# Kernel tuning notes

Hardware: AMD Instinct MI355X
Metric: run time of the kernel (lower is better)

## Reference

```python
import jax, jax.numpy as jnp
import numpy as np

N_NODES = 50000
N_EDGES = 800000
N_GRAPHS = 64


def setup_inputs() -> dict:
    key = jax.random.key(0)
    ks = jax.random.split(key, 12)

    def w(k, shape):
        fan_in = shape[0]
        return jax.random.normal(k, shape, dtype=jnp.float32) / np.sqrt(fan_in)

    x = jax.random.normal(ks[0], (N_NODES, 6), dtype=jnp.float32)
    edge_index = jax.random.randint(ks[1], (2, N_EDGES), 0, N_NODES, dtype=jnp.int64)
    batch = jnp.sort(jax.random.randint(ks[2], (N_NODES,), 0, N_GRAPHS, dtype=jnp.int64))
    return {
        "x": x,
        "edge_index": edge_index,
        "batch": batch,
        "W_in": w(ks[3], (6, 64)),
        "b_in": jnp.zeros((64,), jnp.float32),
        "W1": w(ks[4], (64, 128)),
        "b1": jnp.zeros((128,), jnp.float32),
        "W2": w(ks[5], (128, 128)),
        "b2": jnp.zeros((128,), jnp.float32),
        "Wp": w(ks[6], (256, 256)),
        "bp": jnp.zeros((256,), jnp.float32),
    }


def reference(x, edge_index, batch, W_in, b_in, W1, b1, W2, b2, Wp, bp):
    n = x.shape[0]
    self_loop = jnp.arange(n, dtype=edge_index.dtype)
    src = jnp.concatenate([edge_index[0], self_loop])  # [E+N]
    dst = jnp.concatenate([edge_index[1], self_loop])
    # GCN symmetric normalization with self-loops (PyG GCNConv default)
    deg = jax.ops.segment_sum(jnp.ones_like(dst, x.dtype), dst, num_segments=n)
    dinv = jax.lax.rsqrt(deg)  # deg >= 1 because of self-loops
    norm = (dinv[src] * dinv[dst])[:, None]  # [E+N, 1]

    def gcn(h, W, b):
        hw = h @ W                       # linear first, like GCNConv
        msg = hw[src] * norm             # gather + normalize per edge
        return jax.ops.segment_sum(msg, dst, num_segments=n) + b

    h = x @ W_in + b_in                  # input_projection
    h = jax.nn.relu(gcn(h, W1, b1))      # relu(gnn1(...))
    h = jax.nn.relu(gcn(h, W2, b2))      # relu(gnn2(...))

    # global mean / max pooling over batch segments
    counts = jax.ops.segment_sum(jnp.ones((n,), h.dtype), batch, num_segments=N_GRAPHS)
    h_mean = jax.ops.segment_sum(h, batch, num_segments=N_GRAPHS) / jnp.maximum(counts, 1.0)[:, None]
    h_max = jax.ops.segment_max(h, batch, num_segments=N_GRAPHS)
    h_max = jnp.where(counts[:, None] > 0, h_max, 0.0)
    h_graph = jnp.concatenate([h_mean, h_max], axis=1)  # [G, 256]

    # projection MLP: Linear + ReLU (Dropout is identity in eval)
    return jax.nn.relu(h_graph @ Wp + bp)
```

## Files before the change

### kernel.cpp

```cpp
#include <hip/hip_runtime.h>
#include <hip/hip_fp16.h>

#define N_NODES 50000
#define N_EDGES 800000
#define N_GRAPHS 64
#define N_PAD 50048

#define CB 256
#define EPB (N_EDGES / CB)
#define NBUCKET ((N_NODES + 255) / 256)

typedef _Float16 f16x8 __attribute__((ext_vector_type(8)));
typedef float f32x4 __attribute__((ext_vector_type(4)));

__device__ __forceinline__ unsigned splice2(unsigned z) {
    return ((z & 0x80u) << 8) | ((z & 0x7fu) << 7) |
           ((z & 0x8000u) << 16) | ((z & 0x7f00u) << 15);
}
__device__ __forceinline__ f16x8 dec8(uint2 w) {
    union { unsigned u[4]; f16x8 v; } o;
    o.u[0] = splice2(w.x);
    o.u[1] = splice2(w.x >> 16);
    o.u[2] = splice2(w.y);
    o.u[3] = splice2(w.y >> 16);
    return o.v;
}


__global__ void k_prep(const float* __restrict__ W_in, const float* __restrict__ b_in,
                       const float* __restrict__ W1, const float* __restrict__ W2,
                       _Float16* __restrict__ Wt2, float* __restrict__ Wcz,
                       float* psum, float* pmax, int* totals, int* gcursor,
                       const int* __restrict__ batch, float* __restrict__ pcnt) {
    int idx = blockIdx.x * blockDim.x + threadIdx.x;
    if (idx < 128 * 128) {
        int n = idx >> 7, k = idx & 127;
        Wt2[idx] = (_Float16)(W2[k * 128 + n] * 8.0f);
    } else if (idx < 128 * 128 + 1024) {
        int j = idx - 128 * 128;
        int ch = j >> 3, k = j & 7;
        float acc = 0.f;
        if (k < 6) {
            for (int q = 0; q < 64; q++) acc += W_in[k * 64 + q] * W1[q * 128 + ch];
        } else if (k == 6) {
            for (int q = 0; q < 64; q++) acc += b_in[q] * W1[q * 128 + ch];
        }
        Wcz[k * 128 + ch] = acc;
    }
    if (idx < N_GRAPHS * 128) { psum[idx] = 0.f; pmax[idx] = 0.f; }
    if (idx < 256) { totals[idx] = 0; gcursor[idx] = 0; }
    if (blockIdx.x == 0) {
        __shared__ int shp[N_GRAPHS + 1];
        int tt = threadIdx.x;
        if (tt <= N_GRAPHS) {
            int lo = 0, hi = N_NODES;
            while (lo < hi) {
                int mid = (lo + hi) >> 1;
                if (batch[mid] < tt) lo = mid + 1; else hi = mid;
            }
            shp[tt] = lo;
        }
        __syncthreads();
        if (tt < N_GRAPHS) pcnt[tt] = (float)(shp[tt + 1] - shp[tt]);
    }
}


__global__ __launch_bounds__(256) void k_coarse_hist(const int* __restrict__ dst,
                                                     int* __restrict__ totals) {
    __shared__ int hist[NBUCKET];
    int t = threadIdx.x, b = blockIdx.x;
    for (int i = t; i < NBUCKET; i += 256) hist[i] = 0;
    __syncthreads();
    int e0 = b * EPB;
    for (int e = e0 + t; e < e0 + EPB; e += 256)
        atomicAdd(&hist[dst[e] >> 8], 1);
    __syncthreads();
    for (int i = t; i < NBUCKET; i += 256)
        if (hist[i] > 0) atomicAdd(&totals[i], hist[i]);
}

__global__ __launch_bounds__(256) void k_scan_scatter(
        const int* __restrict__ src, const int* __restrict__ dst,
        const int* __restrict__ totals, int* __restrict__ bucket_base,
        int* __restrict__ gcursor, unsigned int* __restrict__ esort) {
    __shared__ int cur[256];
    __shared__ int sc[256];
    int t = threadIdx.x, b = blockIdx.x;
    cur[t] = 0;
    __syncthreads();
    int e0 = b * EPB;
    for (int e = e0 + t; e < e0 + EPB; e += 256)
        atomicAdd(&cur[dst[e] >> 8], 1);
    __syncthreads();
    int lcnt = cur[t];
    int v = (t < NBUCKET) ? totals[t] : 0;
    sc[t] = v;
    __syncthreads();
    for (int off = 1; off < 256; off <<= 1) {
        int u = (t >= off) ? sc[t - off] : 0;
        __syncthreads();
        sc[t] += u;
        __syncthreads();
    }
    int base = sc[t] - v;
    int off = (t < NBUCKET && lcnt > 0) ? atomicAdd(&gcursor[t], lcnt) : 0;
    cur[t] = base + off;
    if (b == 0) {
        if (t < NBUCKET) bucket_base[t] = base;
        if (t == 0) bucket_base[NBUCKET] = N_EDGES;
    }
    __syncthreads();
    for (int e = e0 + t; e < e0 + EPB; e += 256) {
        int d = dst[e];
        int slot = atomicAdd(&cur[d >> 8], 1);
        esort[slot] = ((unsigned)(d & 255) << 16) | (unsigned)src[e];
    }
}

__global__ __launch_bounds__(256) void k_fine_fill_p(
        const unsigned int* __restrict__ esort, const int* __restrict__ bucket_base,
        int* __restrict__ col, int* __restrict__ row_ptr, float* __restrict__ dinv,
        const float* __restrict__ x, float* __restrict__ p) {
    __shared__ int hist[256];
    __shared__ int sc[256];
    __shared__ int cur[256];
    int t = threadIdx.x, b = blockIdx.x;
    hist[t] = 0;
    __syncthreads();
    int base = bucket_base[b], end = bucket_base[b + 1];
    for (int e = base + t; e < end; e += 256)
        atomicAdd(&hist[(esort[e] >> 16) & 255], 1);
    __syncthreads();
    int v = hist[t];
    sc[t] = v;
    __syncthreads();
    for (int off = 1; off < 256; off <<= 1) {
        int u = (t >= off) ? sc[t - off] : 0;
        __syncthreads();
        sc[t] += u;
        __syncthreads();
    }
    int start = base + sc[t] - v;
    cur[t] = start;
    int node = b * 256 + t;
    float di = rsqrtf((float)(v + 1));
    if (node < N_NODES) {
        row_ptr[node] = start;
        dinv[node] = di;
        float pr[8];
#pragma unroll
        for (int k = 0; k < 6; k++) pr[k] = x[node * 6 + k] * di;
        pr[6] = di;
        pr[7] = 0.f;
        *(f32x4*)&p[(size_t)node * 8] = *(f32x4*)&pr[0];
        *(f32x4*)&p[(size_t)node * 8 + 4] = *(f32x4*)&pr[4];
    }
    if (b == 0 && t == 0) row_ptr[N_NODES] = N_EDGES;
    __syncthreads();
    for (int e = base + t; e < end; e += 256) {
        unsigned pk = esort[e];
        int slot = atomicAdd(&cur[(pk >> 16) & 255], 1);
        col[slot] = (int)(pk & 0xffffu);
    }
}

__global__ __launch_bounds__(256, 8) void k_agg_proj(
        const float* __restrict__ p, const int* __restrict__ row_ptr,
        const int* __restrict__ col, const float* __restrict__ Wcz,
        const float* __restrict__ b1, const float* __restrict__ dinv,
        unsigned char* __restrict__ g1, int n) {
    __shared__ float tl[32][8];
    __shared__ float Wl[8 * 128];
    __shared__ float bl[128];
    int t = threadIdx.x;
    for (int i = t; i < 1024; i += 256) Wl[i] = Wcz[i];
    if (t < 128) bl[t] = b1[t];

    int rg = t >> 3, ck = t & 7;
    int row = blockIdx.x * 32 + rg;
    float acc = 0.f;
    if (row < n) {
        acc = p[(size_t)row * 8 + ck];
        int e = row_ptr[row], e1 = row_ptr[row + 1];
        for (; e + 3 < e1; e += 4) {
            int c0 = col[e], c1 = col[e + 1], c2 = col[e + 2], c3 = col[e + 3];
            float v0 = p[(size_t)c0 * 8 + ck];
            float v1 = p[(size_t)c1 * 8 + ck];
            float v2 = p[(size_t)c2 * 8 + ck];
            float v3 = p[(size_t)c3 * 8 + ck];
            acc += (v0 + v1) + (v2 + v3);
        }
        for (; e < e1; e++) acc += p[(size_t)col[e] * 8 + ck];
    }
    tl[rg][ck] = acc;
    __syncthreads();

    int rg2 = t >> 3, oc = t & 7;
    int row2 = blockIdx.x * 32 + rg2;
    if (row2 < n) {
        float tr[7];
#pragma unroll
        for (int k = 0; k < 7; k++) tr[k] = tl[rg2][k];
        float di = dinv[row2];
        unsigned w[4] = {0u, 0u, 0u, 0u};
#pragma unroll
        for (int c = 0; c < 16; c++) {
            int ch = oc * 16 + c;
            float z = 0.f;
#pragma unroll
            for (int k = 0; k < 7; k++) z += tr[k] * Wl[k * 128 + ch];
            z = di * z + bl[ch];
            float h = fmaxf(z, 0.f) * di;
            union { _Float16 f; unsigned short u; } cv;
            cv.f = (_Float16)(h * 0.125f);
            unsigned hb = cv.u;
            unsigned r = hb & 0x7fffu;
            r = r + 0x3fu + ((r >> 7) & 1u);
            unsigned byte = ((hb >> 8) & 0x80u) | ((r >> 7) & 0x7fu);
            w[c >> 2] |= byte << ((c & 3) * 8);
        }
        *(uint4*)&g1[(size_t)row2 * 128 + oc * 16] = make_uint4(w[0], w[1], w[2], w[3]);
    }
}

__global__ __launch_bounds__(256, 8) void k_gnn2f8(
        const unsigned char* __restrict__ g, const int* __restrict__ row_ptr,
        const int* __restrict__ col, const _Float16* __restrict__ Wt2,
        const float* __restrict__ b2, const float* __restrict__ dinv,
        const int* __restrict__ batch, float* __restrict__ psum,
        float* __restrict__ pmax, int n) {
    constexpr int ROWS = 16, KP = 136;
    __shared__ __align__(16) char smem[ROWS * 128 * 4];
    _Float16* Sl = (_Float16*)smem;
    float* Hs = (float*)smem;
    int t = threadIdx.x;

    {
        int rl = t >> 4, ck = t & 15;
        int row = blockIdx.x * ROWS + rl;
        f16x8 accA = {};
        f16x8 accB = {};
        const uint2* gb = (const uint2*)g;
        if (row < n) {
            accA = dec8(gb[(size_t)row * 16 + ck]);
            int e = row_ptr[row], e1 = row_ptr[row + 1];
            for (; e + 3 < e1; e += 4) {
                int c0 = col[e], c1 = col[e + 1], c2 = col[e + 2], c3 = col[e + 3];
                uint2 v0 = gb[(size_t)c0 * 16 + ck];
                uint2 v1 = gb[(size_t)c1 * 16 + ck];
                uint2 v2 = gb[(size_t)c2 * 16 + ck];
                uint2 v3 = gb[(size_t)c3 * 16 + ck];
                accA += dec8(v0);
                accB += dec8(v1);
                accA += dec8(v2);
                accB += dec8(v3);
            }
            if (e + 1 < e1) {
                uint2 v0 = gb[(size_t)col[e] * 16 + ck];
                uint2 v1 = gb[(size_t)col[e + 1] * 16 + ck];
                accA += dec8(v0);
                accB += dec8(v1);
                e += 2;
            }
            if (e < e1) accA += dec8(gb[(size_t)col[e] * 16 + ck]);
        }
        f16x8 o = accA + accB;
        *(f16x8*)&Sl[rl * KP + ck * 8] = o;
    }
    __syncthreads();

    int wave = t >> 6;
    int lane = t & 63;
    int m = lane & 15;
    int quad = lane >> 4;
    int col_base = wave * 32;

    f32x4 acc[2] = {};
#pragma unroll
    for (int k0 = 0; k0 < 128; k0 += 32) {
        f16x8 a = *(const f16x8*)&Sl[m * KP + k0 + quad * 8];
#pragma unroll
        for (int ct = 0; ct < 2; ct++) {
            f16x8 bw = *(const f16x8*)(Wt2 + (size_t)(col_base + ct * 16 + m) * 128
                                       + k0 + quad * 8);
            acc[ct] = __builtin_amdgcn_mfma_f32_16x16x32_f16(a, bw, acc[ct], 0, 0, 0);
        }
    }

    __syncthreads();
#pragma unroll
    for (int r = 0; r < 4; r++) {
        int rl = quad * 4 + r;
        int row = blockIdx.x * ROWS + rl;
        float di = (row < n) ? dinv[row] : 0.f;
#pragma unroll
        for (int ct = 0; ct < 2; ct++) {
            int colb = col_base + ct * 16 + m;
            float v = fmaxf(di * acc[ct][r] + b2[colb], 0.f);
            Hs[rl * 128 + colb] = (row < n) ? v : 0.f;
        }
    }
    __syncthreads();
    if (t < 128) {
        int colb = t;
        int row0b = blockIdx.x * ROWS;
        float s = 0.f, mx = 0.f;
        int gcur = batch[row0b < n ? row0b : (n - 1)];
        for (int rr = 0; rr < ROWS; rr++) {
            int row = row0b + rr;
            if (row >= n) break;
            int gi = batch[row];
            if (gi != gcur) {
                atomicAdd(&psum[gcur * 128 + colb], s);
                atomicMax((int*)&pmax[gcur * 128 + colb], __float_as_int(mx));
                s = 0.f; mx = 0.f; gcur = gi;
            }
            float v = Hs[rr * 128 + colb];
            s += v;
            mx = fmaxf(mx, v);
        }
        atomicAdd(&psum[gcur * 128 + colb], s);
        atomicMax((int*)&pmax[gcur * 128 + colb], __float_as_int(mx));
    }
}


__global__ void k_final(const float* __restrict__ psum, const float* __restrict__ pmax,
                        const float* __restrict__ pcnt, const float* __restrict__ Wp,
                        const float* __restrict__ bp, float* __restrict__ out) {
    int t = blockIdx.x * blockDim.x + threadIdx.x;
    if (t >= N_GRAPHS * 256) return;
    int g = t >> 8, j = t & 255;
    float inv = 1.0f / fmaxf(pcnt[g], 1.0f);
    float acc = bp[j];
#pragma unroll 4
    for (int k = 0; k < 128; k++) acc += (psum[g * 128 + k] * inv) * Wp[k * 256 + j];
#pragma unroll 4
    for (int k = 0; k < 128; k++) acc += pmax[g * 128 + k] * Wp[(128 + k) * 256 + j];
    out[t] = fmaxf(acc, 0.f);
}

extern "C" void kernel_launch(void* const* d_in, const int* in_sizes, int n_in,
                              void* d_out, int out_size, void* d_ws, size_t ws_size,
                              hipStream_t stream) {
    const int N = N_NODES, E = N_EDGES;
    const float* x    = (const float*)d_in[0];
    const int*   ei   = (const int*)d_in[1];
    const int*   src  = ei;
    const int*   dst  = ei + E;
    const int*   batch= (const int*)d_in[2];
    const float* W_in = (const float*)d_in[3];
    const float* b_in = (const float*)d_in[4];
    const float* W1   = (const float*)d_in[5];
    const float* b1   = (const float*)d_in[6];
    const float* W2   = (const float*)d_in[7];
    const float* b2   = (const float*)d_in[8];
    const float* Wp   = (const float*)d_in[9];
    const float* bp   = (const float*)d_in[10];
    float* out = (float*)d_out;

    char* p8 = (char*)d_ws;
    int* totals      = (int*)p8;   p8 += 256 * 4;
    int* bucket_base = (int*)p8;   p8 += 256 * 4;
    int* gcursor     = (int*)p8;   p8 += 256 * 4;
    int* row_ptr     = (int*)p8;   p8 += (N_PAD + 64) * 4;
    int* col         = (int*)p8;   p8 += (size_t)N_EDGES * 4;
    unsigned* esort  = (unsigned*)p8; p8 += (size_t)N_EDGES * 4;
    float* dinv      = (float*)p8; p8 += N_PAD * 4;
    float* Wcz       = (float*)p8; p8 += 1024 * 4;
    _Float16* Wt2    = (_Float16*)p8; p8 += 128 * 128 * 2;
    float* pfeat     = (float*)p8; p8 += (size_t)N_PAD * 8 * 4;
    unsigned char* g1f8 = (unsigned char*)p8; p8 += (size_t)N_PAD * 128;
    float* psum      = (float*)p8; p8 += N_GRAPHS * 128 * 4;
    float* pmax      = (float*)p8; p8 += N_GRAPHS * 128 * 4;
    float* pcnt      = (float*)p8;

    const int TB = 256;
    dim3 blk(TB);

    k_prep<<<(128 * 128 + 1024 + TB - 1) / TB, blk, 0, stream>>>(
        W_in, b_in, W1, W2, Wt2, Wcz, psum, pmax, totals, gcursor, batch, pcnt);

    k_coarse_hist<<<CB, blk, 0, stream>>>(dst, totals);
    k_scan_scatter<<<CB, blk, 0, stream>>>(src, dst, totals, bucket_base, gcursor, esort);
    k_fine_fill_p<<<NBUCKET, blk, 0, stream>>>(esort, bucket_base, col, row_ptr, dinv,
                                               x, pfeat);

    k_agg_proj<<<(N + 31) / 32, blk, 0, stream>>>(pfeat, row_ptr, col, Wcz, b1, dinv,
                                                  g1f8, N);

    k_gnn2f8<<<(N + 15) / 16, blk, 0, stream>>>(
        g1f8, row_ptr, col, Wt2, b2, dinv, batch, psum, pmax, N);

    k_final<<<(N_GRAPHS * 256 + TB - 1) / TB, blk, 0, stream>>>(psum, pmax, pcnt, Wp, bp, out);
}
```

Baseline: 193.0 us.

## Replace two-pass global edge bucketing with per-block local sort and segment gather

Merges the coarse histogram and scan/scatter kernels into one kernel. Each block sorts its edge chunk by coarse bucket in shared memory, writes it back contiguously, and records per-bucket local offsets. The fine-fill kernel then finds each bucket's segments across all blocks using a prefix scan plus a binary search per edge. This removes one kernel launch, a second pass over dst, the global cursor atomics and scattered global writes, but adds per-edge binary-search overhead and reads from 256 small segments per bucket.

Measured after the change: 202.1 us. 4.7% more time.

```diff
diff --git a/kernel.cpp b/kernel.cpp
--- a/kernel.cpp
+++ b/kernel.cpp
@@ -30,7 +30,7 @@
 __global__ void k_prep(const float* __restrict__ W_in, const float* __restrict__ b_in,
                        const float* __restrict__ W1, const float* __restrict__ W2,
                        _Float16* __restrict__ Wt2, float* __restrict__ Wcz,
-                       float* psum, float* pmax, int* totals, int* gcursor,
+                       float* psum, float* pmax, int* totals,
                        const int* __restrict__ batch, float* __restrict__ pcnt) {
     int idx = blockIdx.x * blockDim.x + threadIdx.x;
     if (idx < 128 * 128) {
@@ -48,7 +48,7 @@
         Wcz[k * 128 + ch] = acc;
     }
     if (idx < N_GRAPHS * 128) { psum[idx] = 0.f; pmax[idx] = 0.f; }
-    if (idx < 256) { totals[idx] = 0; gcursor[idx] = 0; }
+    if (idx < 256) totals[idx] = 0;
     if (blockIdx.x == 0) {
         __shared__ int shp[N_GRAPHS + 1];
         int tt = threadIdx.x;
@@ -65,36 +65,22 @@
     }
 }
 
-
-__global__ __launch_bounds__(256) void k_coarse_hist(const int* __restrict__ dst,
-                                                     int* __restrict__ totals) {
-    __shared__ int hist[NBUCKET];
+__global__ __launch_bounds__(256) void k_lsort(
+        const int* __restrict__ src, const int* __restrict__ dst,
+        int* __restrict__ totals, unsigned int* __restrict__ esort,
+        int* __restrict__ lstart) {
+    __shared__ int hist[256];
+    __shared__ int sc[256];
+    __shared__ int cur[256];
+    __shared__ unsigned stage[EPB];
     int t = threadIdx.x, b = blockIdx.x;
-    for (int i = t; i < NBUCKET; i += 256) hist[i] = 0;
+    hist[t] = 0;
     __syncthreads();
     int e0 = b * EPB;
     for (int e = e0 + t; e < e0 + EPB; e += 256)
         atomicAdd(&hist[dst[e] >> 8], 1);
     __syncthreads();
-    for (int i = t; i < NBUCKET; i += 256)
-        if (hist[i] > 0) atomicAdd(&totals[i], hist[i]);
-}
-
-__global__ __launch_bounds__(256) void k_scan_scatter(
-        const int* __restrict__ src, const int* __restrict__ dst,
-        const int* __restrict__ totals, int* __restrict__ bucket_base,
-        int* __restrict__ gcursor, unsigned int* __restrict__ esort) {
-    __shared__ int cur[256];
-    __shared__ int sc[256];
-    int t = threadIdx.x, b = blockIdx.x;
-    cur[t] = 0;
-    __syncthreads();
-    int e0 = b * EPB;
-    for (int e = e0 + t; e < e0 + EPB; e += 256)
-        atomicAdd(&cur[dst[e] >> 8], 1);
-    __syncthreads();
-    int lcnt = cur[t];
-    int v = (t < NBUCKET) ? totals[t] : 0;
+    int v = hist[t];
     sc[t] = v;
     __syncthreads();
     for (int off = 1; off < 256; off <<= 1) {
@@ -104,33 +90,74 @@
         __syncthreads();
     }
     int base = sc[t] - v;
-    int off = (t < NBUCKET && lcnt > 0) ? atomicAdd(&gcursor[t], lcnt) : 0;
-    cur[t] = base + off;
-    if (b == 0) {
-        if (t < NBUCKET) bucket_base[t] = base;
-        if (t == 0) bucket_base[NBUCKET] = N_EDGES;
-    }
+    cur[t] = base;
+    if (t < NBUCKET) {
+        lstart[t * 256 + b] = base;
+        if (v > 0) atomicAdd(&totals[t], v);
+    }
+    if (t == 0) lstart[NBUCKET * 256 + b] = EPB;
     __syncthreads();
     for (int e = e0 + t; e < e0 + EPB; e += 256) {
         int d = dst[e];
         int slot = atomicAdd(&cur[d >> 8], 1);
-        esort[slot] = ((unsigned)(d & 255) << 16) | (unsigned)src[e];
-    }
+        stage[slot] = ((unsigned)(d & 255) << 16) | (unsigned)src[e];
+    }
+    __syncthreads();
+    for (int i = t; i < EPB; i += 256)
+        esort[e0 + i] = stage[i];
 }
 
 __global__ __launch_bounds__(256) void k_fine_fill_p(
-        const unsigned int* __restrict__ esort, const int* __restrict__ bucket_base,
-        int* __restrict__ col, int* __restrict__ row_ptr, float* __restrict__ dinv,
+        const unsigned int* __restrict__ esort, const int* __restrict__ lstart,
+        const int* __restrict__ totals, int* __restrict__ col,
+        int* __restrict__ row_ptr, float* __restrict__ dinv,
         const float* __restrict__ x, float* __restrict__ p) {
     __shared__ int hist[256];
     __shared__ int sc[256];
     __shared__ int cur[256];
-    int t = threadIdx.x, b = blockIdx.x;
+    __shared__ int segls[256];
+    __shared__ int segoff[257];
+    __shared__ int bb0;
+    int t = threadIdx.x, i = blockIdx.x;
+
+    int tv = (t < NBUCKET) ? totals[t] : 0;
+    sc[t] = tv;
+    __syncthreads();
+    for (int off = 1; off < 256; off <<= 1) {
+        int u = (t >= off) ? sc[t - off] : 0;
+        __syncthreads();
+        sc[t] += u;
+        __syncthreads();
+    }
+    if (t == i) bb0 = sc[t] - tv;
+    int ls = lstart[i * 256 + t];
+    int cnt = lstart[(i + 1) * 256 + t] - ls;
+    segls[t] = ls;
+    __syncthreads();
+    sc[t] = cnt;
+    __syncthreads();
+    for (int off = 1; off < 256; off <<= 1) {
+        int u = (t >= off) ? sc[t - off] : 0;
+        __syncthreads();
+        sc[t] += u;
+        __syncthreads();
+    }
+    segoff[t + 1] = sc[t];
+    if (t == 0) segoff[0] = 0;
     hist[t] = 0;
     __syncthreads();
-    int base = bucket_base[b], end = bucket_base[b + 1];
-    for (int e = base + t; e < end; e += 256)
-        atomicAdd(&hist[(esort[e] >> 16) & 255], 1);
+    int base = bb0;
+    int total = segoff[256];
+
+    for (int e = t; e < total; e += 256) {
+        int lo = 0, hi = 256;
+        while (hi - lo > 1) {
+            int mid = (lo + hi) >> 1;
+            if (e >= segoff[mid]) lo = mid; else hi = mid;
+        }
+        unsigned pk = esort[lo * EPB + segls[lo] + (e - segoff[lo])];
+        atomicAdd(&hist[(pk >> 16) & 255], 1);
+    }
     __syncthreads();
     int v = hist[t];
     sc[t] = v;
@@ -143,7 +170,7 @@
     }
     int start = base + sc[t] - v;
     cur[t] = start;
-    int node = b * 256 + t;
+    int node = i * 256 + t;
     float di = rsqrtf((float)(v + 1));
     if (node < N_NODES) {
         row_ptr[node] = start;
@@ -156,10 +183,16 @@
         *(f32x4*)&p[(size_t)node * 8] = *(f32x4*)&pr[0];
         *(f32x4*)&p[(size_t)node * 8 + 4] = *(f32x4*)&pr[4];
     }
-    if (b == 0 && t == 0) row_ptr[N_NODES] = N_EDGES;
-    __syncthreads();
-    for (int e = base + t; e < end; e += 256) {
-        unsigned pk = esort[e];
+    if (i == 0 && t == 0) row_ptr[N_NODES] = N_EDGES;
+    __syncthreads();
+
+    for (int e = t; e < total; e += 256) {
+        int lo = 0, hi = 256;
+        while (hi - lo > 1) {
+            int mid = (lo + hi) >> 1;
+            if (e >= segoff[mid]) lo = mid; else hi = mid;
+        }
+        unsigned pk = esort[lo * EPB + segls[lo] + (e - segoff[lo])];
         int slot = atomicAdd(&cur[(pk >> 16) & 255], 1);
         col[slot] = (int)(pk & 0xffffu);
     }
@@ -362,8 +395,7 @@
 
     char* p8 = (char*)d_ws;
     int* totals      = (int*)p8;   p8 += 256 * 4;
-    int* bucket_base = (int*)p8;   p8 += 256 * 4;
-    int* gcursor     = (int*)p8;   p8 += 256 * 4;
+    int* lstart      = (int*)p8;   p8 += 197 * 256 * 4;
     int* row_ptr     = (int*)p8;   p8 += (N_PAD + 64) * 4;
     int* col         = (int*)p8;   p8 += (size_t)N_EDGES * 4;
     unsigned* esort  = (unsigned*)p8; p8 += (size_t)N_EDGES * 4;
@@ -380,12 +412,11 @@
     dim3 blk(TB);
 
     k_prep<<<(128 * 128 + 1024 + TB - 1) / TB, blk, 0, stream>>>(
-        W_in, b_in, W1, W2, Wt2, Wcz, psum, pmax, totals, gcursor, batch, pcnt);
-
-    k_coarse_hist<<<CB, blk, 0, stream>>>(dst, totals);
-    k_scan_scatter<<<CB, blk, 0, stream>>>(src, dst, totals, bucket_base, gcursor, esort);
-    k_fine_fill_p<<<NBUCKET, blk, 0, stream>>>(esort, bucket_base, col, row_ptr, dinv,
-                                               x, pfeat);
+        W_in, b_in, W1, W2, Wt2, Wcz, psum, pmax, totals, batch, pcnt);
+
+    k_lsort<<<CB, blk, 0, stream>>>(src, dst, totals, esort, lstart);
+    k_fine_fill_p<<<NBUCKET, blk, 0, stream>>>(esort, lstart, totals, col, row_ptr,
+                                               dinv, x, pfeat);
 
     k_agg_proj<<<(N + 31) / 32, blk, 0, stream>>>(pfeat, row_ptr, col, Wcz, b1, dinv,
                                                   g1f8, N);
```
